# Kernel optimization log

Hardware: AMD Instinct MI355X
Metric: run time of the kernel (lower is better)

The kernel has to match this reference:

```python
import jax, jax.numpy as jnp
import numpy as np

N_NODES = 100000
N_EDGES = 600000
D = 128
H = 256


def setup_inputs() -> dict:
    key = jax.random.key(0)
    ks = jax.random.split(key, 8)
    nodes = jax.random.normal(ks[0], (N_NODES, D), dtype=jnp.float32)
    senders = jax.random.randint(ks[1], (N_EDGES,), 0, N_NODES)
    receivers = jax.random.randint(ks[2], (N_EDGES,), 0, N_NODES)
    s = 0.05
    return {
        "nodes": nodes,
        "senders": senders,
        "receivers": receivers,
        "Wm1": jax.random.normal(ks[3], (D, H), dtype=jnp.float32) * s,
        "bm1": jnp.zeros((H,), dtype=jnp.float32),
        "Wm2": jax.random.normal(ks[4], (H, D), dtype=jnp.float32) * s,
        "bm2": jnp.zeros((D,), dtype=jnp.float32),
        "Wn1": jax.random.normal(ks[5], (2 * D, H), dtype=jnp.float32) * s,
        "bn1": jnp.zeros((H,), dtype=jnp.float32),
        "Wn2": jax.random.normal(ks[6], (H, D), dtype=jnp.float32) * s,
        "bn2": jnp.zeros((D,), dtype=jnp.float32),
    }


def reference(nodes, senders, receivers, Wm1, bm1, Wm2, bm2, Wn1, bn1, Wn2, bn2):
    # message MLP applied per node (vmap(message_fn) over nodes)
    m = jax.nn.relu(nodes @ Wm1 + bm1) @ Wm2 + bm2            # [N, D]
    # gather messages along edges by sender, segment_sum to receivers
    agg = jax.ops.segment_sum(m[senders], receivers, num_segments=nodes.shape[0])  # [N, D]
    # node update MLP on [nodes || aggregated messages]
    h = jnp.concatenate([nodes, agg], axis=-1)                # [N, 2D]
    upd = jax.nn.relu(h @ Wn1 + bn1) @ Wn2 + bn2              # [N, D]
    # residual add
    return nodes + upd
```

## Files before the change

### kernel.cpp

```cpp
#include <hip/hip_runtime.h>
#include <hip/hip_bf16.h>

#define NN 100000
#define DD 128
#define HH 256
#define NE 600000
#define CAP 32

typedef short bf8 __attribute__((ext_vector_type(8)));
typedef float f32x4 __attribute__((ext_vector_type(4)));
typedef unsigned short u16x8 __attribute__((ext_vector_type(8)));

__device__ __forceinline__ unsigned short f2bf(float f) {
  unsigned int u = __builtin_bit_cast(unsigned int, f);
  u += 0x7fffu + ((u >> 16) & 1u);
  return (unsigned short)(u >> 16);
}
__device__ __forceinline__ float bf2f(unsigned short h) {
  unsigned int u = ((unsigned int)h) << 16;
  return __builtin_bit_cast(float, u);
}

__global__ __launch_bounds__(256) void prep(
    const float* __restrict__ Wm1, const float* __restrict__ Wm2,
    const float* __restrict__ Wn1, const float* __restrict__ Wn2,
    unsigned short* __restrict__ Pm1, unsigned short* __restrict__ Pm2,
    unsigned short* __restrict__ Pn1, unsigned short* __restrict__ Pn2,
    int* __restrict__ cnt) {
  int b = blockIdx.x;
  for (int i = b * 256 + threadIdx.x; i < NN; i += 80 * 256) cnt[i] = 0;

  const float* W; unsigned short* P; int K, N, base;
  if (b < 16)      { W = Wm1; P = Pm1; K = 128; N = 256; base = 0;  }
  else if (b < 32) { W = Wm2; P = Pm2; K = 256; N = 128; base = 16; }
  else if (b < 64) { W = Wn1; P = Pn1; K = 256; N = 256; base = 32; }
  else             { W = Wn2; P = Pn2; K = 256; N = 128; base = 64; }
  int idx = (b - base) * 256 + threadIdx.x;
  int KT = K >> 5;
  int lane = idx & 63;
  int t = idx >> 6;
  int kt = t % KT, nt = t / KT;
  int n = nt * 16 + (lane & 15);
  int k0 = kt * 32 + (lane >> 4) * 8;
  unsigned short* dst = P + (size_t)idx * 8;
#pragma unroll
  for (int j = 0; j < 8; ++j) dst[j] = f2bf(W[(size_t)(k0 + j) * N + n]);
}

__global__ __launch_bounds__(256) void fill_buckets(
    const int* __restrict__ snd, const int* __restrict__ rcv,
    int* __restrict__ cnt, int* __restrict__ ebuf) {
  int e = blockIdx.x * 256 + threadIdx.x;
  if (e >= NE) return;
  int r = rcv[e];
  int pos = atomicAdd(&cnt[r], 1);
  if (pos < CAP) ebuf[r * CAP + pos] = snd[e];
}

__global__ __launch_bounds__(256) void msg_mlp(
    const float* __restrict__ nodes, unsigned short* __restrict__ Xb,
    const unsigned short* __restrict__ W1p, const float* __restrict__ b1,
    const unsigned short* __restrict__ W2p, const float* __restrict__ b2,
    unsigned short* __restrict__ Mb) {
  __shared__ __align__(16) unsigned short h[64][264];
  const int row0 = blockIdx.x * 64;
  const int tid = threadIdx.x;
  const int lane = tid & 63, wave = tid >> 6;
  const int l15 = lane & 15, l4 = lane >> 4;

#pragma unroll
  for (int i = 0; i < 8; ++i) {
    int flat = (i * 256 + tid) * 4;
    int r = flat >> 7, c = flat & 127;
    float4 v = make_float4(0.f, 0.f, 0.f, 0.f);
    bool ok = (row0 + r < NN);
    if (ok) v = *(const float4*)(nodes + (size_t)(row0 + r) * DD + c);
    ushort4 o;
    o.x = f2bf(v.x); o.y = f2bf(v.y); o.z = f2bf(v.z); o.w = f2bf(v.w);
    *(ushort4*)&h[r][c] = o;
    if (ok) *(ushort4*)(Xb + (size_t)(row0 + r) * DD + c) = o;
  }
  __syncthreads();

  f32x4 acc[4][4];
#pragma unroll
  for (int mt = 0; mt < 4; ++mt)
#pragma unroll
    for (int nt = 0; nt < 4; ++nt) acc[mt][nt] = (f32x4){0.f, 0.f, 0.f, 0.f};
#pragma unroll
  for (int kt = 0; kt < 4; ++kt) {
    bf8 wfr[4], xfr[4];
#pragma unroll
    for (int mt = 0; mt < 4; ++mt) {
      int Htile = wave * 4 + mt;
      wfr[mt] = *(const bf8*)(W1p + ((size_t)(Htile * 4 + kt) * 64 + lane) * 8);
    }
#pragma unroll
    for (int nt = 0; nt < 4; ++nt)
      xfr[nt] = *(const bf8*)&h[nt * 16 + l15][kt * 32 + l4 * 8];
#pragma unroll
    for (int mt = 0; mt < 4; ++mt)
#pragma unroll
      for (int nt = 0; nt < 4; ++nt)
        acc[mt][nt] = __builtin_amdgcn_mfma_f32_16x16x32_bf16(wfr[mt], xfr[nt], acc[mt][nt], 0, 0, 0);
  }
  __syncthreads();

#pragma unroll
  for (int mt = 0; mt < 4; ++mt) {
    int Hbase = wave * 64 + mt * 16 + l4 * 4;
    float4 bv = *(const float4*)(b1 + Hbase);
#pragma unroll
    for (int nt = 0; nt < 4; ++nt) {
      ushort4 o;
      float v0 = acc[mt][nt][0] + bv.x; o.x = f2bf(v0 > 0.f ? v0 : 0.f);
      float v1 = acc[mt][nt][1] + bv.y; o.y = f2bf(v1 > 0.f ? v1 : 0.f);
      float v2 = acc[mt][nt][2] + bv.z; o.z = f2bf(v2 > 0.f ? v2 : 0.f);
      float v3 = acc[mt][nt][3] + bv.w; o.w = f2bf(v3 > 0.f ? v3 : 0.f);
      *(ushort4*)&h[nt * 16 + l15][Hbase] = o;
    }
  }
  __syncthreads();

  f32x4 acc2[2][4];
#pragma unroll
  for (int mt = 0; mt < 2; ++mt)
#pragma unroll
    for (int nt = 0; nt < 4; ++nt) acc2[mt][nt] = (f32x4){0.f, 0.f, 0.f, 0.f};
#pragma unroll
  for (int kt = 0; kt < 8; ++kt) {
    bf8 wfr[2], xfr[4];
#pragma unroll
    for (int mt = 0; mt < 2; ++mt) {
      int Dtile = wave * 2 + mt;
      wfr[mt] = *(const bf8*)(W2p + ((size_t)(Dtile * 8 + kt) * 64 + lane) * 8);
    }
#pragma unroll
    for (int nt = 0; nt < 4; ++nt)
      xfr[nt] = *(const bf8*)&h[nt * 16 + l15][kt * 32 + l4 * 8];
#pragma unroll
    for (int mt = 0; mt < 2; ++mt)
#pragma unroll
      for (int nt = 0; nt < 4; ++nt)
        acc2[mt][nt] = __builtin_amdgcn_mfma_f32_16x16x32_bf16(wfr[mt], xfr[nt], acc2[mt][nt], 0, 0, 0);
  }
#pragma unroll
  for (int mt = 0; mt < 2; ++mt) {
    int Dbase = wave * 32 + mt * 16 + l4 * 4;
    float4 bv = *(const float4*)(b2 + Dbase);
#pragma unroll
    for (int nt = 0; nt < 4; ++nt) {
      int node = row0 + nt * 16 + l15;
      if (node < NN) {
        ushort4 o;
        o.x = f2bf(acc2[mt][nt][0] + bv.x);
        o.y = f2bf(acc2[mt][nt][1] + bv.y);
        o.z = f2bf(acc2[mt][nt][2] + bv.z);
        o.w = f2bf(acc2[mt][nt][3] + bv.w);
        *(ushort4*)(Mb + (size_t)node * DD + Dbase) = o;
      }
    }
  }
}

__global__ __launch_bounds__(256) void gather(
    const unsigned short* __restrict__ Mb, const int* __restrict__ ebuf,
    const int* __restrict__ cnt, unsigned short* __restrict__ aggb) {
  int node = blockIdx.x * 4 + (threadIdx.x >> 6);
  if (node >= NN) return;
  int lane = threadIdx.x & 63;
  int deg = cnt[node];
  deg = (deg < CAP) ? deg : CAP;
  const int base_e = node * CAP;
  float a0 = 0.f, a1 = 0.f;
  for (int b = 0; b < deg; b += 8) {
    int s[8];
    ushort2 mv[8];
#pragma unroll
    for (int u = 0; u < 8; ++u) s[u] = ebuf[base_e + b + u];
#pragma unroll
    for (int u = 0; u < 8; ++u) {
      int sl = s[u];
      sl = (sl < 0) ? 0 : sl;
      sl = (sl >= NN) ? 0 : sl;
      mv[u] = *(const ushort2*)(Mb + (size_t)sl * DD + lane * 2);
    }
#pragma unroll
    for (int u = 0; u < 8; ++u) {
      bool act = (b + u) < deg;
      a0 += act ? bf2f(mv[u].x) : 0.f;
      a1 += act ? bf2f(mv[u].y) : 0.f;
    }
  }
  ushort2 o;
  o.x = f2bf(a0);
  o.y = f2bf(a1);
  *(ushort2*)(aggb + (size_t)node * DD + lane * 2) = o;
}

__global__ __launch_bounds__(256) void node_mlp(
    const unsigned short* __restrict__ Xb, const unsigned short* __restrict__ aggb,
    const unsigned short* __restrict__ W1p, const float* __restrict__ b1,
    const unsigned short* __restrict__ W2p, const float* __restrict__ b2,
    float* __restrict__ out) {
  __shared__ __align__(16) unsigned short h[64][264];
  const int row0 = blockIdx.x * 64;
  const int tid = threadIdx.x;
  const int lane = tid & 63, wave = tid >> 6;
  const int l15 = lane & 15, l4 = lane >> 4;

#pragma unroll
  for (int i = 0; i < 4; ++i) {
    int flat = (i * 256 + tid) * 8;
    int r = flat >> 7, c = flat & 127;
    u16x8 v = (u16x8)0;
    if (row0 + r < NN) v = *(const u16x8*)(Xb + (size_t)(row0 + r) * DD + c);
    *(u16x8*)&h[r][c] = v;
  }
#pragma unroll
  for (int i = 0; i < 4; ++i) {
    int flat = (i * 256 + tid) * 8;
    int r = flat >> 7, c = flat & 127;
    u16x8 v = (u16x8)0;
    if (row0 + r < NN) v = *(const u16x8*)(aggb + (size_t)(row0 + r) * DD + c);
    *(u16x8*)&h[r][128 + c] = v;
  }
  __syncthreads();

  ushort4 resid[2][4];
#pragma unroll
  for (int mt = 0; mt < 2; ++mt) {
    int Dbase = wave * 32 + mt * 16 + l4 * 4;
#pragma unroll
    for (int nt = 0; nt < 4; ++nt)
      resid[mt][nt] = *(ushort4*)&h[nt * 16 + l15][Dbase];
  }

  f32x4 acc[4][4];
#pragma unroll
  for (int mt = 0; mt < 4; ++mt)
#pragma unroll
    for (int nt = 0; nt < 4; ++nt) acc[mt][nt] = (f32x4){0.f, 0.f, 0.f, 0.f};
#pragma unroll
  for (int kt = 0; kt < 8; ++kt) {
    bf8 wfr[4], xfr[4];
#pragma unroll
    for (int mt = 0; mt < 4; ++mt) {
      int Htile = wave * 4 + mt;
      wfr[mt] = *(const bf8*)(W1p + ((size_t)(Htile * 8 + kt) * 64 + lane) * 8);
    }
#pragma unroll
    for (int nt = 0; nt < 4; ++nt)
      xfr[nt] = *(const bf8*)&h[nt * 16 + l15][kt * 32 + l4 * 8];
#pragma unroll
    for (int mt = 0; mt < 4; ++mt)
#pragma unroll
      for (int nt = 0; nt < 4; ++nt)
        acc[mt][nt] = __builtin_amdgcn_mfma_f32_16x16x32_bf16(wfr[mt], xfr[nt], acc[mt][nt], 0, 0, 0);
  }
  __syncthreads();

#pragma unroll
  for (int mt = 0; mt < 4; ++mt) {
    int Hbase = wave * 64 + mt * 16 + l4 * 4;
    float4 bv = *(const float4*)(b1 + Hbase);
#pragma unroll
    for (int nt = 0; nt < 4; ++nt) {
      ushort4 o;
      float v0 = acc[mt][nt][0] + bv.x; o.x = f2bf(v0 > 0.f ? v0 : 0.f);
      float v1 = acc[mt][nt][1] + bv.y; o.y = f2bf(v1 > 0.f ? v1 : 0.f);
      float v2 = acc[mt][nt][2] + bv.z; o.z = f2bf(v2 > 0.f ? v2 : 0.f);
      float v3 = acc[mt][nt][3] + bv.w; o.w = f2bf(v3 > 0.f ? v3 : 0.f);
      *(ushort4*)&h[nt * 16 + l15][Hbase] = o;
    }
  }
  __syncthreads();

  f32x4 acc2[2][4];
#pragma unroll
  for (int mt = 0; mt < 2; ++mt)
#pragma unroll
    for (int nt = 0; nt < 4; ++nt) acc2[mt][nt] = (f32x4){0.f, 0.f, 0.f, 0.f};
#pragma unroll
  for (int kt = 0; kt < 8; ++kt) {
    bf8 wfr[2], xfr[4];
#pragma unroll
    for (int mt = 0; mt < 2; ++mt) {
      int Dtile = wave * 2 + mt;
      wfr[mt] = *(const bf8*)(W2p + ((size_t)(Dtile * 8 + kt) * 64 + lane) * 8);
    }
#pragma unroll
    for (int nt = 0; nt < 4; ++nt)
      xfr[nt] = *(const bf8*)&h[nt * 16 + l15][kt * 32 + l4 * 8];
#pragma unroll
    for (int mt = 0; mt < 2; ++mt)
#pragma unroll
      for (int nt = 0; nt < 4; ++nt)
        acc2[mt][nt] = __builtin_amdgcn_mfma_f32_16x16x32_bf16(wfr[mt], xfr[nt], acc2[mt][nt], 0, 0, 0);
  }
#pragma unroll
  for (int mt = 0; mt < 2; ++mt) {
    int Dbase = wave * 32 + mt * 16 + l4 * 4;
    float4 bv = *(const float4*)(b2 + Dbase);
#pragma unroll
    for (int nt = 0; nt < 4; ++nt) {
      int node = row0 + nt * 16 + l15;
      if (node < NN) {
        float4 o;
        o.x = bf2f(resid[mt][nt].x) + acc2[mt][nt][0] + bv.x;
        o.y = bf2f(resid[mt][nt].y) + acc2[mt][nt][1] + bv.y;
        o.z = bf2f(resid[mt][nt].z) + acc2[mt][nt][2] + bv.z;
        o.w = bf2f(resid[mt][nt].w) + acc2[mt][nt][3] + bv.w;
        *(float4*)(out + (size_t)node * DD + Dbase) = o;
      }
    }
  }
}

extern "C" void kernel_launch(void* const* d_in, const int* in_sizes, int n_in,
                              void* d_out, int out_size, void* d_ws, size_t ws_size,
                              hipStream_t stream) {
  const float* nodes = (const float*)d_in[0];
  const int* senders = (const int*)d_in[1];
  const int* receivers = (const int*)d_in[2];
  const float* Wm1 = (const float*)d_in[3];
  const float* bm1 = (const float*)d_in[4];
  const float* Wm2 = (const float*)d_in[5];
  const float* bm2 = (const float*)d_in[6];
  const float* Wn1 = (const float*)d_in[7];
  const float* bn1 = (const float*)d_in[8];
  const float* Wn2 = (const float*)d_in[9];
  const float* bn2 = (const float*)d_in[10];
  float* out = (float*)d_out;

  char* ws = (char*)d_ws;
  unsigned short* Xb   = (unsigned short*)(ws);
  unsigned short* Mb   = (unsigned short*)(ws + 25600000);
  unsigned short* aggb = (unsigned short*)(ws + 51200000);
  int* cnt    = (int*)(ws + 76800000);
  int* ebuf   = (int*)(ws + 77200000);
  unsigned short* Wm1p = (unsigned short*)(ws + 90000000);
  unsigned short* Wm2p = (unsigned short*)(ws + 90065536);
  unsigned short* Wn1p = (unsigned short*)(ws + 90131072);
  unsigned short* Wn2p = (unsigned short*)(ws + 90262144);

  prep<<<80, 256, 0, stream>>>(Wm1, Wm2, Wn1, Wn2, Wm1p, Wm2p, Wn1p, Wn2p, cnt);
  fill_buckets<<<(NE + 255) / 256, 256, 0, stream>>>(senders, receivers, cnt, ebuf);
  msg_mlp<<<1563, 256, 0, stream>>>(nodes, Xb, Wm1p, bm1, Wm2p, bm2, Mb);
  gather<<<25000, 256, 0, stream>>>(Mb, ebuf, cnt, aggb);
  node_mlp<<<1563, 256, 0, stream>>>(Xb, aggb, Wn1p, bn1, Wn2p, bn2, out);
}
```

Before: 256.5 us.

## Fuse edge bucketing into message MLP and use 512-thread MLP blocks

The separate fill_buckets kernel is folded into msg_mlp, with each block bucketing 512 edges before its MLP work. This removes one launch and lets the atomic scatter overlap with the GEMM. Both MLP kernels now run 8 waves per 64-row tile instead of 4, so each wave owns fewer output tiles. That lowers per-wave register use and raises the number of waves available to hide latency, but each block now loads the weights through more waves and the edge atomics add contention inside the MLP kernel.

Measured after the change: 242.7 us. 1.06x faster.

```diff
diff --git a/kernel.cpp b/kernel.cpp
--- a/kernel.cpp
+++ b/kernel.cpp
@@ -47,30 +47,31 @@
   for (int j = 0; j < 8; ++j) dst[j] = f2bf(W[(size_t)(k0 + j) * N + n]);
 }
 
-__global__ __launch_bounds__(256) void fill_buckets(
-    const int* __restrict__ snd, const int* __restrict__ rcv,
-    int* __restrict__ cnt, int* __restrict__ ebuf) {
-  int e = blockIdx.x * 256 + threadIdx.x;
-  if (e >= NE) return;
-  int r = rcv[e];
-  int pos = atomicAdd(&cnt[r], 1);
-  if (pos < CAP) ebuf[r * CAP + pos] = snd[e];
-}
-
-__global__ __launch_bounds__(256) void msg_mlp(
+__global__ __launch_bounds__(512) void msg_mlp(
     const float* __restrict__ nodes, unsigned short* __restrict__ Xb,
     const unsigned short* __restrict__ W1p, const float* __restrict__ b1,
     const unsigned short* __restrict__ W2p, const float* __restrict__ b2,
-    unsigned short* __restrict__ Mb) {
+    unsigned short* __restrict__ Mb,
+    const int* __restrict__ snd, const int* __restrict__ rcv,
+    int* __restrict__ cnt, int* __restrict__ ebuf) {
   __shared__ __align__(16) unsigned short h[64][264];
   const int row0 = blockIdx.x * 64;
   const int tid = threadIdx.x;
   const int lane = tid & 63, wave = tid >> 6;
   const int l15 = lane & 15, l4 = lane >> 4;
 
-#pragma unroll
-  for (int i = 0; i < 8; ++i) {
-    int flat = (i * 256 + tid) * 4;
+  {
+    int e = blockIdx.x * 512 + tid;
+    if (e < NE) {
+      int r = rcv[e];
+      int pos = atomicAdd(&cnt[r], 1);
+      if (pos < CAP) ebuf[r * CAP + pos] = snd[e];
+    }
+  }
+
+#pragma unroll
+  for (int i = 0; i < 4; ++i) {
+    int flat = (i * 512 + tid) * 4;
     int r = flat >> 7, c = flat & 127;
     float4 v = make_float4(0.f, 0.f, 0.f, 0.f);
     bool ok = (row0 + r < NN);
@@ -82,24 +83,24 @@
   }
   __syncthreads();
 
-  f32x4 acc[4][4];
-#pragma unroll
-  for (int mt = 0; mt < 4; ++mt)
+  f32x4 acc[2][4];
+#pragma unroll
+  for (int mt = 0; mt < 2; ++mt)
 #pragma unroll
     for (int nt = 0; nt < 4; ++nt) acc[mt][nt] = (f32x4){0.f, 0.f, 0.f, 0.f};
 #pragma unroll
   for (int kt = 0; kt < 4; ++kt) {
-    bf8 wfr[4], xfr[4];
-#pragma unroll
-    for (int mt = 0; mt < 4; ++mt) {
-      int Htile = wave * 4 + mt;
+    bf8 wfr[2], xfr[4];
+#pragma unroll
+    for (int mt = 0; mt < 2; ++mt) {
+      int Htile = wave * 2 + mt;
       wfr[mt] = *(const bf8*)(W1p + ((size_t)(Htile * 4 + kt) * 64 + lane) * 8);
     }
 #pragma unroll
     for (int nt = 0; nt < 4; ++nt)
       xfr[nt] = *(const bf8*)&h[nt * 16 + l15][kt * 32 + l4 * 8];
 #pragma unroll
-    for (int mt = 0; mt < 4; ++mt)
+    for (int mt = 0; mt < 2; ++mt)
 #pragma unroll
       for (int nt = 0; nt < 4; ++nt)
         acc[mt][nt] = __builtin_amdgcn_mfma_f32_16x16x32_bf16(wfr[mt], xfr[nt], acc[mt][nt], 0, 0, 0);
@@ -107,8 +108,8 @@
   __syncthreads();
 
 #pragma unroll
-  for (int mt = 0; mt < 4; ++mt) {
-    int Hbase = wave * 64 + mt * 16 + l4 * 4;
+  for (int mt = 0; mt < 2; ++mt) {
+    int Hbase = wave * 32 + mt * 16 + l4 * 4;
     float4 bv = *(const float4*)(b1 + Hbase);
 #pragma unroll
     for (int nt = 0; nt < 4; ++nt) {
@@ -122,41 +123,32 @@
   }
   __syncthreads();
 
-  f32x4 acc2[2][4];
-#pragma unroll
-  for (int mt = 0; mt < 2; ++mt)
-#pragma unroll
-    for (int nt = 0; nt < 4; ++nt) acc2[mt][nt] = (f32x4){0.f, 0.f, 0.f, 0.f};
+  f32x4 acc2[4];
+#pragma unroll
+  for (int nt = 0; nt < 4; ++nt) acc2[nt] = (f32x4){0.f, 0.f, 0.f, 0.f};
 #pragma unroll
   for (int kt = 0; kt < 8; ++kt) {
-    bf8 wfr[2], xfr[4];
-#pragma unroll
-    for (int mt = 0; mt < 2; ++mt) {
-      int Dtile = wave * 2 + mt;
-      wfr[mt] = *(const bf8*)(W2p + ((size_t)(Dtile * 8 + kt) * 64 + lane) * 8);
-    }
+    bf8 wfr, xfr[4];
+    wfr = *(const bf8*)(W2p + ((size_t)(wave * 8 + kt) * 64 + lane) * 8);
 #pragma unroll
     for (int nt = 0; nt < 4; ++nt)
       xfr[nt] = *(const bf8*)&h[nt * 16 + l15][kt * 32 + l4 * 8];
 #pragma unroll
-    for (int mt = 0; mt < 2; ++mt)
-#pragma unroll
-      for (int nt = 0; nt < 4; ++nt)
-        acc2[mt][nt] = __builtin_amdgcn_mfma_f32_16x16x32_bf16(wfr[mt], xfr[nt], acc2[mt][nt], 0, 0, 0);
-  }
-#pragma unroll
-  for (int mt = 0; mt < 2; ++mt) {
-    int Dbase = wave * 32 + mt * 16 + l4 * 4;
+    for (int nt = 0; nt < 4; ++nt)
+      acc2[nt] = __builtin_amdgcn_mfma_f32_16x16x32_bf16(wfr, xfr[nt], acc2[nt], 0, 0, 0);
+  }
+  {
+    int Dbase = wave * 16 + l4 * 4;
     float4 bv = *(const float4*)(b2 + Dbase);
 #pragma unroll
     for (int nt = 0; nt < 4; ++nt) {
       int node = row0 + nt * 16 + l15;
       if (node < NN) {
         ushort4 o;
-        o.x = f2bf(acc2[mt][nt][0] + bv.x);
-        o.y = f2bf(acc2[mt][nt][1] + bv.y);
-        o.z = f2bf(acc2[mt][nt][2] + bv.z);
-        o.w = f2bf(acc2[mt][nt][3] + bv.w);
+        o.x = f2bf(acc2[nt][0] + bv.x);
+        o.y = f2bf(acc2[nt][1] + bv.y);
+        o.z = f2bf(acc2[nt][2] + bv.z);
+        o.w = f2bf(acc2[nt][3] + bv.w);
         *(ushort4*)(Mb + (size_t)node * DD + Dbase) = o;
       }
     }
@@ -198,7 +190,7 @@
   *(ushort2*)(aggb + (size_t)node * DD + lane * 2) = o;
 }
 
-__global__ __launch_bounds__(256) void node_mlp(
+__global__ __launch_bounds__(512) void node_mlp(
     const unsigned short* __restrict__ Xb, const unsigned short* __restrict__ aggb,
     const unsigned short* __restrict__ W1p, const float* __restrict__ b1,
     const unsigned short* __restrict__ W2p, const float* __restrict__ b2,
@@ -210,16 +202,16 @@
   const int l15 = lane & 15, l4 = lane >> 4;
 
 #pragma unroll
-  for (int i = 0; i < 4; ++i) {
-    int flat = (i * 256 + tid) * 8;
+  for (int i = 0; i < 2; ++i) {
+    int flat = (i * 512 + tid) * 8;
     int r = flat >> 7, c = flat & 127;
     u16x8 v = (u16x8)0;
     if (row0 + r < NN) v = *(const u16x8*)(Xb + (size_t)(row0 + r) * DD + c);
     *(u16x8*)&h[r][c] = v;
   }
 #pragma unroll
-  for (int i = 0; i < 4; ++i) {
-    int flat = (i * 256 + tid) * 8;
+  for (int i = 0; i < 2; ++i) {
+    int flat = (i * 512 + tid) * 8;
     int r = flat >> 7, c = flat & 127;
     u16x8 v = (u16x8)0;
     if (row0 + r < NN) v = *(const u16x8*)(aggb + (size_t)(row0 + r) * DD + c);
@@ -227,33 +219,32 @@
   }
   __syncthreads();
 
-  ushort4 resid[2][4];
-#pragma unroll
-  for (int mt = 0; mt < 2; ++mt) {
-    int Dbase = wave * 32 + mt * 16 + l4 * 4;
-#pragma unroll
-    for (int nt = 0; nt < 4; ++nt)
-      resid[mt][nt] = *(ushort4*)&h[nt * 16 + l15][Dbase];
-  }
-
-  f32x4 acc[4][4];
-#pragma unroll
-  for (int mt = 0; mt < 4; ++mt)
+  ushort4 resid[4];
+  {
+    int Dbase = wave * 16 + l4 * 4;
+#pragma unroll
+    for (int nt = 0; nt < 4; ++nt)
+      resid[nt] = *(ushort4*)&h[nt * 16 + l15][Dbase];
+  }
+
+  f32x4 acc[2][4];
+#pragma unroll
+  for (int mt = 0; mt < 2; ++mt)
 #pragma unroll
     for (int nt = 0; nt < 4; ++nt) acc[mt][nt] = (f32x4){0.f, 0.f, 0.f, 0.f};
 #pragma unroll
   for (int kt = 0; kt < 8; ++kt) {
-    bf8 wfr[4], xfr[4];
-#pragma unroll
-    for (int mt = 0; mt < 4; ++mt) {
-      int Htile = wave * 4 + mt;
+    bf8 wfr[2], xfr[4];
+#pragma unroll
+    for (int mt = 0; mt < 2; ++mt) {
+      int Htile = wave * 2 + mt;
       wfr[mt] = *(const bf8*)(W1p + ((size_t)(Htile * 8 + kt) * 64 + lane) * 8);
     }
 #pragma unroll
     for (int nt = 0; nt < 4; ++nt)
       xfr[nt] = *(const bf8*)&h[nt * 16 + l15][kt * 32 + l4 * 8];
 #pragma unroll
-    for (int mt = 0; mt < 4; ++mt)
+    for (int mt = 0; mt < 2; ++mt)
 #pragma unroll
       for (int nt = 0; nt < 4; ++nt)
         acc[mt][nt] = __builtin_amdgcn_mfma_f32_16x16x32_bf16(wfr[mt], xfr[nt], acc[mt][nt], 0, 0, 0);
@@ -261,8 +252,8 @@
   __syncthreads();
 
 #pragma unroll
-  for (int mt = 0; mt < 4; ++mt) {
-    int Hbase = wave * 64 + mt * 16 + l4 * 4;
+  for (int mt = 0; mt < 2; ++mt) {
+    int Hbase = wave * 32 + mt * 16 + l4 * 4;
     float4 bv = *(const float4*)(b1 + Hbase);
 #pragma unroll
     for (int nt = 0; nt < 4; ++nt) {
@@ -276,41 +267,32 @@
   }
   __syncthreads();
 
-  f32x4 acc2[2][4];
-#pragma unroll
-  for (int mt = 0; mt < 2; ++mt)
-#pragma unroll
-    for (int nt = 0; nt < 4; ++nt) acc2[mt][nt] = (f32x4){0.f, 0.f, 0.f, 0.f};
+  f32x4 acc2[4];
+#pragma unroll
+  for (int nt = 0; nt < 4; ++nt) acc2[nt] = (f32x4){0.f, 0.f, 0.f, 0.f};
 #pragma unroll
   for (int kt = 0; kt < 8; ++kt) {
-    bf8 wfr[2], xfr[4];
-#pragma unroll
-    for (int mt = 0; mt < 2; ++mt) {
-      int Dtile = wave * 2 + mt;
-      wfr[mt] = *(const bf8*)(W2p + ((size_t)(Dtile * 8 + kt) * 64 + lane) * 8);
-    }
+    bf8 wfr, xfr[4];
+    wfr = *(const bf8*)(W2p + ((size_t)(wave * 8 + kt) * 64 + lane) * 8);
 #pragma unroll
     for (int nt = 0; nt < 4; ++nt)
       xfr[nt] = *(const bf8*)&h[nt * 16 + l15][kt * 32 + l4 * 8];
 #pragma unroll
-    for (int mt = 0; mt < 2; ++mt)
-#pragma unroll
-      for (int nt = 0; nt < 4; ++nt)
-        acc2[mt][nt] = __builtin_amdgcn_mfma_f32_16x16x32_bf16(wfr[mt], xfr[nt], acc2[mt][nt], 0, 0, 0);
-  }
-#pragma unroll
-  for (int mt = 0; mt < 2; ++mt) {
-    int Dbase = wave * 32 + mt * 16 + l4 * 4;
+    for (int nt = 0; nt < 4; ++nt)
+      acc2[nt] = __builtin_amdgcn_mfma_f32_16x16x32_bf16(wfr, xfr[nt], acc2[nt], 0, 0, 0);
+  }
+  {
+    int Dbase = wave * 16 + l4 * 4;
     float4 bv = *(const float4*)(b2 + Dbase);
 #pragma unroll
     for (int nt = 0; nt < 4; ++nt) {
       int node = row0 + nt * 16 + l15;
       if (node < NN) {
         float4 o;
-        o.x = bf2f(resid[mt][nt].x) + acc2[mt][nt][0] + bv.x;
-        o.y = bf2f(resid[mt][nt].y) + acc2[mt][nt][1] + bv.y;
-        o.z = bf2f(resid[mt][nt].z) + acc2[mt][nt][2] + bv.z;
-        o.w = bf2f(resid[mt][nt].w) + acc2[mt][nt][3] + bv.w;
+        o.x = bf2f(resid[nt].x) + acc2[nt][0] + bv.x;
+        o.y = bf2f(resid[nt].y) + acc2[nt][1] + bv.y;
+        o.z = bf2f(resid[nt].z) + acc2[nt][2] + bv.z;
+        o.w = bf2f(resid[nt].w) + acc2[nt][3] + bv.w;
         *(float4*)(out + (size_t)node * DD + Dbase) = o;
       }
     }
@@ -345,8 +327,8 @@
   unsigned short* Wn2p = (unsigned short*)(ws + 90262144);
 
   prep<<<80, 256, 0, stream>>>(Wm1, Wm2, Wn1, Wn2, Wm1p, Wm2p, Wn1p, Wn2p, cnt);
-  fill_buckets<<<(NE + 255) / 256, 256, 0, stream>>>(senders, receivers, cnt, ebuf);
-  msg_mlp<<<1563, 256, 0, stream>>>(nodes, Xb, Wm1p, bm1, Wm2p, bm2, Mb);
+  msg_mlp<<<1563, 512, 0, stream>>>(nodes, Xb, Wm1p, bm1, Wm2p, bm2, Mb,
+                                    senders, receivers, cnt, ebuf);
   gather<<<25000, 256, 0, stream>>>(Mb, ebuf, cnt, aggb);
-  node_mlp<<<1563, 256, 0, stream>>>(Xb, aggb, Wn1p, bn1, Wn2p, bn2, out);
-}
+  node_mlp<<<1563, 512, 0, stream>>>(Xb, aggb, Wn1p, bn1, Wn2p, bn2, out);
+}
```
